# Optimization experiments

Hardware: AMD Instinct MI355X
Metric: run time of the kernel (lower is better)

## Reference

```python
import jax, jax.numpy as jnp
import numpy as np

H = W = 512
MAX_ID = 15          # instance ids 1..15 (0 = background)
N_SIGMA = 1
FG_WEIGHT = 1.0
W_INST, W_VAR, W_SEED = 1.0, 10.0, 1.0


def make_xym(h, w):
    # channel 0 varies along width (x), channel 1 along height (y), like the torch buffer
    xs = jnp.linspace(0.0, 1.0, 512)
    xm = jnp.broadcast_to(xs[None, None, :], (1, 512, 512))
    ym = jnp.broadcast_to(xs[None, :, None], (1, 512, 512))
    xym = jnp.concatenate([xm, ym], axis=0)
    return xym[:, :h, :w]


def lovasz_hinge_flat(logits, labels):
    # logits, labels: flat [P]; labels in {0,1} float
    signs = 2.0 * labels - 1.0
    errors = 1.0 - logits * signs
    perm = jnp.argsort(-errors)                 # descending
    errors_sorted = errors[perm]
    gt_sorted = labels[perm]
    gts = jnp.sum(gt_sorted)
    intersection = gts - jnp.cumsum(gt_sorted)
    union = gts + jnp.cumsum(1.0 - gt_sorted)
    jaccard = 1.0 - intersection / union
    jaccard = jnp.concatenate([jaccard[:1], jaccard[1:] - jaccard[:-1]])
    return jnp.sum(jax.nn.relu(errors_sorted) * jaccard)


def _per_image(pred_b, inst_b, lab_b, xym):
    spatial_emb = jnp.tanh(pred_b[0:2]) + xym          # (2,H,W)
    sigma = pred_b[2]                                  # (H,W), n_sigma=1
    seed_map = jax.nn.sigmoid(pred_b[3])               # (H,W)

    bg = (lab_b == 0)
    seed_bg = jnp.sum(jnp.where(bg, seed_map ** 2, 0.0))

    def per_inst(iid):
        m = (inst_b == iid).astype(pred_b.dtype)       # (H,W)
        cnt = jnp.sum(m)
        present = cnt > 0
        cnt_s = jnp.maximum(cnt, 1.0)
        # to_center=True: center from coordinate map
        center = jnp.sum(xym * m[None], axis=(1, 2)) / cnt_s            # (2,)
        sig_mean = jnp.sum(sigma * m) / cnt_s
        var_l = jnp.sum((sigma - jax.lax.stop_gradient(sig_mean)) ** 2 * m) / cnt_s
        s = jnp.exp(sig_mean * 10.0)
        d2 = jnp.sum((spatial_emb - center[:, None, None]) ** 2, axis=0)  # (H,W)
        dist = jnp.exp(-d2 * s)
        inst_l = lovasz_hinge_flat(dist.reshape(-1) * 2.0 - 1.0, m.reshape(-1))
        seed_l = jnp.sum((seed_map - jax.lax.stop_gradient(dist)) ** 2 * m)
        intra_l = 1.0 - jnp.sum(dist * m) / cnt_s
        return present, var_l, inst_l, seed_l, intra_l

    ids = jnp.arange(1, MAX_ID + 1)
    present, var_l, inst_l, seed_l, intra_l = jax.vmap(per_inst)(ids)
    pf = present.astype(pred_b.dtype)
    obj = jnp.sum(pf)
    obj_s = jnp.maximum(obj, 1.0)
    instance_loss = jnp.sum(inst_l * pf) / obj_s
    var_loss = jnp.sum(var_l * pf) / obj_s
    intra_loss = jnp.sum(intra_l * pf)          # NOT divided by obj_count (as in source)
    seed_loss = (seed_bg + FG_WEIGHT * jnp.sum(seed_l * pf)) / (H * W)
    return W_INST * instance_loss + W_VAR * var_loss + W_SEED * seed_loss + 5.0 * intra_loss


def setup_inputs() -> dict:
    key = jax.random.key(0)
    k1, k2, k3 = jax.random.split(key, 3)
    prediction = jax.random.normal(k1, (4, 4, H, W), dtype=jnp.float32)
    instances = jax.random.randint(k2, (4, H, W), 0, MAX_ID + 1, dtype=jnp.int32)
    labels = jax.random.randint(k3, (4, H, W), 0, 2, dtype=jnp.int32)
    return {"prediction": prediction, "instances": instances, "labels": labels}


def reference(prediction, instances, labels):
    xym = make_xym(prediction.shape[2], prediction.shape[3])
    per_b = jax.vmap(_per_image, in_axes=(0, 0, 0, None))(prediction, instances, labels, xym)
    return jnp.mean(per_b)
```

## Files before the change

kernel.cpp:

```cpp
#include <hip/hip_runtime.h>

#define HW     262144
#define NB     4
#define NID    15
#define KB     256
#define CHUNKS 128
#define PXC    (HW / CHUNKS)

#define WS_STATR  0
#define WS_SEEDBG 1024
#define WS_ACCR   1028
#define WS_LOV    1796
#define WS_CTRL   2048
#define WS_HIST   2048
#define HIST_U32  (NB * CHUNKS * NID * KB)
#define WS_EMBX   (WS_HIST + HIST_U32)
#define MAP_SZ    (NB * HW)
#define WS_EMBY   (WS_EMBX + MAP_SZ)
#define WS_SEEDM  (WS_EMBY + MAP_SZ)
#define WS_TOTAL  (WS_SEEDM + MAP_SZ)

__device__ __forceinline__ float rcp_fast(float x) { return __builtin_amdgcn_rcpf(x); }
__device__ __forceinline__ float fast_tanh(float x) {
    return 1.0f - 2.0f * rcp_fast(__expf(2.0f * x) + 1.0f);
}
__device__ __forceinline__ float fast_sigmoid(float x) {
    return rcp_fast(1.0f + __expf(-x));
}

__global__ __launch_bounds__(256) void zeroKernel(float* __restrict__ ws) {
    ws[blockIdx.x * 256 + threadIdx.x] = 0.f;
}

__global__ __launch_bounds__(256) void prepKernel(const float* __restrict__ pred,
                                                  const int* __restrict__ inst,
                                                  const int* __restrict__ lab,
                                                  float* __restrict__ ws) {
    __shared__ float s_acc[16][68];
    const int b   = blockIdx.y;
    const int tid = threadIdx.x;
    for (int j = tid; j < 16 * 68; j += 256) ((float*)s_acc)[j] = 0.f;
    __syncthreads();

    const int grp = tid >> 4;
    const int ib = b * HW;
    const float* p0 = pred + (((size_t)(b * 4 + 0)) << 18);
    const float* p1 = pred + (((size_t)(b * 4 + 1)) << 18);
    const float* p2 = pred + (((size_t)(b * 4 + 2)) << 18);
    const float* p3 = pred + (((size_t)(b * 4 + 3)) << 18);
    float* embx  = ws + WS_EMBX + ib;
    float* emby  = ws + WS_EMBY + ib;
    float* seedm = ws + WS_SEEDM + ib;
    const float inv511 = 1.0f / 511.0f;

    const int p = blockIdx.x * 1024 + tid * 4;
    const int4   i4 = *(const int4*)(inst + ib + p);
    const int4   l4 = *(const int4*)(lab + ib + p);
    const float4 a4 = *(const float4*)(p0 + p);
    const float4 b4 = *(const float4*)(p1 + p);
    const float4 g4 = *(const float4*)(p2 + p);
    const float4 t4 = *(const float4*)(p3 + p);
    const float xs0 = (float)(p & 511) * inv511;
    const float ys  = (float)(p >> 9) * inv511;

    float4 ex, ey, sd;
    ex.x = fast_tanh(a4.x) + xs0;
    ex.y = fast_tanh(a4.y) + xs0 + inv511;
    ex.z = fast_tanh(a4.z) + xs0 + 2.f * inv511;
    ex.w = fast_tanh(a4.w) + xs0 + 3.f * inv511;
    ey.x = fast_tanh(b4.x) + ys;
    ey.y = fast_tanh(b4.y) + ys;
    ey.z = fast_tanh(b4.z) + ys;
    ey.w = fast_tanh(b4.w) + ys;
    sd.x = fast_sigmoid(t4.x);
    sd.y = fast_sigmoid(t4.y);
    sd.z = fast_sigmoid(t4.z);
    sd.w = fast_sigmoid(t4.w);
    *(float4*)(embx + p)  = ex;
    *(float4*)(emby + p)  = ey;
    *(float4*)(seedm + p) = sd;

    float sbg = 0.f;
    sbg += (l4.x == 0) ? sd.x * sd.x : 0.f;
    sbg += (l4.y == 0) ? sd.y * sd.y : 0.f;
    sbg += (l4.z == 0) ? sd.z * sd.z : 0.f;
    sbg += (l4.w == 0) ? sd.w * sd.w : 0.f;

#define ACC_PX(IID, XS, SG)                                   \
    if ((IID) > 0) {                                          \
        float* a = &s_acc[grp][((IID) - 1) * 4];              \
        atomicAdd(a + 0, 1.f);                                \
        atomicAdd(a + 1, (XS));                               \
        atomicAdd(a + 2, ys);                                 \
        atomicAdd(a + 3, (SG));                               \
    }
    ACC_PX(i4.x, xs0, g4.x)
    ACC_PX(i4.y, xs0 + inv511, g4.y)
    ACC_PX(i4.z, xs0 + 2.f * inv511, g4.z)
    ACC_PX(i4.w, xs0 + 3.f * inv511, g4.w)
#undef ACC_PX

#pragma unroll
    for (int m = 32; m; m >>= 1) sbg += __shfl_xor(sbg, m, 64);
    if ((tid & 63) == 0) atomicAdd(&s_acc[grp][60], sbg);
    __syncthreads();

    if (tid < 61) {
        float tot = 0.f;
#pragma unroll
        for (int q = 0; q < 16; ++q) tot += s_acc[q][tid];
        if (tid < 60) atomicAdd(ws + WS_STATR + (blockIdx.x & 3) * 256 + b * 60 + tid, tot);
        else          atomicAdd(ws + WS_SEEDBG + b, tot);
    }
}

#define HCOPY_STRIDE (NID * KB + 1)
__global__ __launch_bounds__(256) void histKernel(const float* __restrict__ pred,
                                                  const int* __restrict__ inst,
                                                  float* __restrict__ ws) {
    __shared__ unsigned s_hist[4 * HCOPY_STRIDE];
    __shared__ float4   s_stat4[NID];
    __shared__ float    s_facc[8][48];

    const int b     = blockIdx.y;
    const int chunk = blockIdx.x;
    const int tid   = threadIdx.x;

    if (tid < NID) {
        float cnt = 0.f, sx = 0.f, sy = 0.f, ss = 0.f;
#pragma unroll
        for (int r = 0; r < 4; ++r) {
            const float* st = ws + WS_STATR + r * 256 + b * 60 + tid * 4;
            cnt += st[0]; sx += st[1]; sy += st[2]; ss += st[3];
        }
        float ic = rcp_fast(fmaxf(cnt, 1.f));
        float sigm = ss * ic;
        s_stat4[tid] = make_float4(sx * ic, sy * ic, sigm, __expf(10.f * sigm));
    }
    for (int j = tid; j < 4 * HCOPY_STRIDE; j += 256) s_hist[j] = 0u;
    for (int j = tid; j < 8 * 48; j += 256) ((float*)s_facc)[j] = 0.f;
    __syncthreads();

    float csx[NID], csy[NID], css[NID];
#pragma unroll
    for (int i = 0; i < NID; ++i) {
        float4 v = s_stat4[i];
        csx[i] = v.x; csy[i] = v.y; css[i] = v.w;
    }

    unsigned* myhist = &s_hist[((tid >> 4) & 3) * HCOPY_STRIDE];
    float* myfacc = s_facc[(tid >> 3) & 7];
    const int ib = b * HW;
    const float* sig   = pred + (((size_t)(b * 4 + 2)) << 18);
    const float* embx  = ws + WS_EMBX + ib;
    const float* emby  = ws + WS_EMBY + ib;
    const float* seedm = ws + WS_SEEDM + ib;

    auto doPx = [&](float exv, float eyv, float sdv, float gv, int iid) {
#pragma unroll
        for (int i = 0; i < NID; ++i) {
            float dx = exv - csx[i], dy = eyv - csy[i];
            float dist = __expf(-(dx * dx + dy * dy) * css[i]);
            float u1 = dist * (float)KB;
            bool m = (iid == i + 1);
            float bf = m ? ((float)KB - u1) : u1;
            int bk = min((int)bf, KB - 1);
            atomicAdd(&myhist[i * KB + bk], m ? 1u : 0x10000u);
        }
        if (iid > 0) {
            float4 st = s_stat4[iid - 1];
            float dx = exv - st.x, dy = eyv - st.y;
            float dist = __expf(-(dx * dx + dy * dy) * st.w);
            float dsg = gv - st.z;
            float e2 = sdv - dist;
            float* fa = &myfacc[(iid - 1) * 3];
            atomicAdd(fa + 0, dsg * dsg);
            atomicAdd(fa + 1, e2 * e2);
            atomicAdd(fa + 2, dist);
        }
    };

#pragma unroll
    for (int u = 0; u < 2; ++u) {
        const int p = chunk * PXC + u * 1024 + tid * 4;
        const int4   i4 = *(const int4*)(inst + ib + p);
        const float4 exq = *(const float4*)(embx + p);
        const float4 eyq = *(const float4*)(emby + p);
        const float4 sdq = *(const float4*)(seedm + p);
        const float4 gq  = *(const float4*)(sig + p);
        doPx(exq.x, eyq.x, sdq.x, gq.x, i4.x);
        doPx(exq.y, eyq.y, sdq.y, gq.y, i4.y);
        doPx(exq.z, eyq.z, sdq.z, gq.z, i4.z);
        doPx(exq.w, eyq.w, sdq.w, gq.w, i4.w);
    }
    __syncthreads();

    unsigned* dst = (unsigned*)(ws + WS_HIST) + (size_t)(b * CHUNKS + chunk) * (NID * KB);
    for (int j = tid; j < NID * KB; j += 256) {
        dst[j] = s_hist[j] + s_hist[HCOPY_STRIDE + j] +
                 s_hist[2 * HCOPY_STRIDE + j] + s_hist[3 * HCOPY_STRIDE + j];
    }

    if (tid < 45) {
        float tot = 0.f;
#pragma unroll
        for (int q = 0; q < 8; ++q) tot += s_facc[q][tid];
        atomicAdd(ws + WS_ACCR + (chunk & 3) * 192 + b * 48 + tid, tot);
    }
}

__global__ __launch_bounds__(256) void lovaszKernel(float* __restrict__ ws) {
    __shared__ unsigned s_pf[4][KB];
    __shared__ unsigned s_pb[4][KB];
    const int t = blockIdx.x;
    const int b = t / NID, i = t % NID;
    const int tid = threadIdx.x, wv = tid >> 6, lane = tid & 63;

    float G = 0.f;
#pragma unroll
    for (int r = 0; r < 4; ++r) G += ws[WS_STATR + r * 256 + b * 60 + i * 4];

    if (G > 0.f) {
        unsigned af0 = 0, af1 = 0, af2 = 0, af3 = 0;
        unsigned ab0 = 0, ab1 = 0, ab2 = 0, ab3 = 0;
        const unsigned* histU = (const unsigned*)(ws + WS_HIST);
        for (int k = 0; k < 32; ++k) {
            const int c = wv * 32 + k;
            const unsigned* hb = histU + ((size_t)(b * CHUNKS + c) * NID + i) * KB + lane * 4;
            uint4 q = *(const uint4*)hb;
            af0 += q.x & 0xffffu; ab0 += q.x >> 16;
            af1 += q.y & 0xffffu; ab1 += q.y >> 16;
            af2 += q.z & 0xffffu; ab2 += q.z >> 16;
            af3 += q.w & 0xffffu; ab3 += q.w >> 16;
        }
        s_pf[wv][lane * 4 + 0] = af0; s_pb[wv][lane * 4 + 0] = ab0;
        s_pf[wv][lane * 4 + 1] = af1; s_pb[wv][lane * 4 + 1] = ab1;
        s_pf[wv][lane * 4 + 2] = af2; s_pb[wv][lane * 4 + 2] = ab2;
        s_pf[wv][lane * 4 + 3] = af3; s_pb[wv][lane * 4 + 3] = ab3;
    }
    __syncthreads();

    float sum = 0.f;
    if (wv == 0 && G > 0.f) {
        float fgs[4], bgs[4];
#pragma unroll
        for (int q = 0; q < 4; ++q) {
            int k = lane * 4 + q;
            fgs[q] = (float)(s_pf[0][k] + s_pf[1][k] + s_pf[2][k] + s_pf[3][k]);
            bgs[q] = (float)(s_pb[0][k] + s_pb[1][k] + s_pb[2][k] + s_pb[3][k]);
        }
        float Fl = fgs[0] + fgs[1] + fgs[2] + fgs[3];
        float Bl = bgs[0] + bgs[1] + bgs[2] + bgs[3];
        float Fs = Fl, Bs = Bl;
#pragma unroll
        for (int d = 1; d < 64; d <<= 1) {
            float fu = __shfl_down(Fs, d, 64);
            float bu = __shfl_down(Bs, d, 64);
            if (lane + d < 64) { Fs += fu; Bs += bu; }
        }
        float F = Fs - Fl, B = Bs - Bl;
        float Jprev = 1.f - (G - F) * rcp_fast(G + B);
        const float ew = 2.f / (float)KB;
#pragma unroll
        for (int q = 3; q >= 0; --q) {
            F += fgs[q]; B += bgs[q];
            float J = 1.f - (G - F) * rcp_fast(G + B);
            float ek = ((float)(lane * 4 + q) + 0.5f) * ew;
            sum += ek * (J - Jprev);
            Jprev = J;
        }
#pragma unroll
        for (int m = 32; m; m >>= 1) sum += __shfl_xor(sum, m, 64);
    }
    if (tid == 0) ws[WS_LOV + t] = sum;
}

__global__ __launch_bounds__(64) void finalKernel(const float* __restrict__ ws,
                                                  float* __restrict__ out) {
    __shared__ float s_c[60][5];
    const int tid = threadIdx.x;
    if (tid < 60) {
        const int b = tid / NID, i = tid % NID;
        float cnt = 0.f, v = 0.f, sdl = 0.f, dm = 0.f;
#pragma unroll
        for (int r = 0; r < 4; ++r) {
            cnt += ws[WS_STATR + r * 256 + b * 60 + i * 4];
            const float* ac = ws + WS_ACCR + r * 192 + b * 48 + i * 3;
            v += ac[0]; sdl += ac[1]; dm += ac[2];
        }
        float pf = cnt > 0.f ? 1.f : 0.f;
        float ic = cnt > 0.f ? 1.f / cnt : 0.f;
        s_c[tid][0] = pf;
        s_c[tid][1] = pf * ws[WS_LOV + tid];
        s_c[tid][2] = pf * v * ic;
        s_c[tid][3] = pf * (1.f - dm * ic);
        s_c[tid][4] = pf * sdl;
    }
    __syncthreads();
    if (tid == 0) {
        float total = 0.f;
        for (int b = 0; b < NB; ++b) {
            float obj = 0.f, instl = 0.f, varl = 0.f, intral = 0.f, seedl = 0.f;
            for (int i = 0; i < NID; ++i) {
                const float* r = s_c[b * NID + i];
                obj += r[0]; instl += r[1]; varl += r[2]; intral += r[3]; seedl += r[4];
            }
            float objs = fmaxf(obj, 1.f);
            total += instl / objs
                   + 10.f * (varl / objs)
                   + (ws[WS_SEEDBG + b] + seedl) / (float)HW
                   + 5.f * intral;
        }
        out[0] = total * 0.25f;
    }
}

extern "C" void kernel_launch(void* const* d_in, const int* in_sizes, int n_in,
                              void* d_out, int out_size, void* d_ws, size_t ws_size,
                              hipStream_t stream) {
    const float* pred = (const float*)d_in[0];
    const int*   inst = (const int*)d_in[1];
    const int*   lab  = (const int*)d_in[2];
    float* ws  = (float*)d_ws;
    float* out = (float*)d_out;

    zeroKernel<<<WS_CTRL / 256, 256, 0, stream>>>(ws);
    prepKernel<<<dim3(256, NB), 256, 0, stream>>>(pred, inst, lab, ws);
    histKernel<<<dim3(CHUNKS, NB), 256, 0, stream>>>(pred, inst, ws);
    lovaszKernel<<<60, 256, 0, stream>>>(ws);
    finalKernel<<<1, 64, 0, stream>>>(ws, out);
}
```

Measured before the change: 79.68 us.

## Drop zero and final kernels via per-block partials and last-block ticket

Replaces the global float atomics into zeroed accumulators with per-block partial writes. Each consumer now reduces those partials itself, which removes the separate zeroing kernel. The final reduction is folded into the Lovasz kernel: a ticket counter picks the last block to compute the output, cutting two kernel launches. It adds redundant partial-sum reads in every hist block and depends on threadfence-based cross-block ordering.

```diff
diff --git a/kernel.cpp b/kernel.cpp
--- a/kernel.cpp
+++ b/kernel.cpp
@@ -7,12 +7,13 @@
 #define CHUNKS 128
 #define PXC    (HW / CHUNKS)
 
-#define WS_STATR  0
-#define WS_SEEDBG 1024
-#define WS_ACCR   1028
-#define WS_LOV    1796
-#define WS_CTRL   2048
-#define WS_HIST   2048
+#define WS_TICKET 0
+#define WS_GACC   4
+#define WS_SBGR   24
+#define WS_PART   64
+#define PART_STR  1024
+#define WS_FACC   65600
+#define WS_HIST   90432
 #define HIST_U32  (NB * CHUNKS * NID * KB)
 #define WS_EMBX   (WS_HIST + HIST_U32)
 #define MAP_SZ    (NB * HW)
@@ -27,10 +28,7 @@
 __device__ __forceinline__ float fast_sigmoid(float x) {
     return rcp_fast(1.0f + __expf(-x));
 }
-
-__global__ __launch_bounds__(256) void zeroKernel(float* __restrict__ ws) {
-    ws[blockIdx.x * 256 + threadIdx.x] = 0.f;
-}
+__device__ __forceinline__ float atomic_read(float* p) { return atomicAdd(p, 0.0f); }
 
 __global__ __launch_bounds__(256) void prepKernel(const float* __restrict__ pred,
                                                   const int* __restrict__ inst,
@@ -109,8 +107,11 @@
         float tot = 0.f;
 #pragma unroll
         for (int q = 0; q < 16; ++q) tot += s_acc[q][tid];
-        if (tid < 60) atomicAdd(ws + WS_STATR + (blockIdx.x & 3) * 256 + b * 60 + tid, tot);
-        else          atomicAdd(ws + WS_SEEDBG + b, tot);
+        ws[WS_PART + tid * PART_STR + b * 256 + blockIdx.x] = tot;
+    }
+    if (blockIdx.x == 0 && b == 0) {
+        if (tid < 20)       ws[WS_GACC + tid] = 0.f;
+        else if (tid == 20) ((unsigned*)ws)[WS_TICKET] = 0u;
     }
 }
 
@@ -121,24 +122,32 @@
     __shared__ unsigned s_hist[4 * HCOPY_STRIDE];
     __shared__ float4   s_stat4[NID];
     __shared__ float    s_facc[8][48];
+    __shared__ float    s_comp[61];
 
     const int b     = blockIdx.y;
     const int chunk = blockIdx.x;
     const int tid   = threadIdx.x;
-
-    if (tid < NID) {
-        float cnt = 0.f, sx = 0.f, sy = 0.f, ss = 0.f;
-#pragma unroll
-        for (int r = 0; r < 4; ++r) {
-            const float* st = ws + WS_STATR + r * 256 + b * 60 + tid * 4;
-            cnt += st[0]; sx += st[1]; sy += st[2]; ss += st[3];
-        }
-        float ic = rcp_fast(fmaxf(cnt, 1.f));
-        float sigm = ss * ic;
-        s_stat4[tid] = make_float4(sx * ic, sy * ic, sigm, __expf(10.f * sigm));
+    const int wv = tid >> 6, lane = tid & 63;
+
+    for (int c = wv; c < 61; c += 4) {
+        const float* pp = ws + WS_PART + c * PART_STR + b * 256;
+        float v = pp[lane] + pp[lane + 64] + pp[lane + 128] + pp[lane + 192];
+#pragma unroll
+        for (int m = 32; m; m >>= 1) v += __shfl_xor(v, m, 64);
+        if (lane == 0) s_comp[c] = v;
     }
     for (int j = tid; j < 4 * HCOPY_STRIDE; j += 256) s_hist[j] = 0u;
     for (int j = tid; j < 8 * 48; j += 256) ((float*)s_facc)[j] = 0.f;
+    __syncthreads();
+
+    if (tid < NID) {
+        float cnt = s_comp[tid * 4 + 0];
+        float ic = rcp_fast(fmaxf(cnt, 1.f));
+        float sigm = s_comp[tid * 4 + 3] * ic;
+        s_stat4[tid] = make_float4(s_comp[tid * 4 + 1] * ic, s_comp[tid * 4 + 2] * ic,
+                                   sigm, __expf(10.f * sigm));
+    }
+    if (chunk == 0 && tid == 16) ws[WS_SBGR + b] = s_comp[60];
     __syncthreads();
 
     float csx[NID], csy[NID], css[NID];
@@ -200,25 +209,46 @@
         dst[j] = s_hist[j] + s_hist[HCOPY_STRIDE + j] +
                  s_hist[2 * HCOPY_STRIDE + j] + s_hist[3 * HCOPY_STRIDE + j];
     }
-
     if (tid < 45) {
         float tot = 0.f;
 #pragma unroll
         for (int q = 0; q < 8; ++q) tot += s_facc[q][tid];
-        atomicAdd(ws + WS_ACCR + (chunk & 3) * 192 + b * 48 + tid, tot);
-    }
-}
-
-__global__ __launch_bounds__(256) void lovaszKernel(float* __restrict__ ws) {
+        ws[WS_FACC + (size_t)(b * CHUNKS + chunk) * 48 + tid] = tot;
+    }
+}
+
+__global__ __launch_bounds__(256) void lovaszKernel(float* __restrict__ ws,
+                                                    float* __restrict__ out) {
     __shared__ unsigned s_pf[4][KB];
     __shared__ unsigned s_pb[4][KB];
+    __shared__ float s4[4];
+    __shared__ float s_f[4][3];
     const int t = blockIdx.x;
     const int b = t / NID, i = t % NID;
     const int tid = threadIdx.x, wv = tid >> 6, lane = tid & 63;
 
-    float G = 0.f;
-#pragma unroll
-    for (int r = 0; r < 4; ++r) G += ws[WS_STATR + r * 256 + b * 60 + i * 4];
+    {
+        float g = ws[WS_PART + (i * 4) * PART_STR + b * 256 + tid];
+#pragma unroll
+        for (int m = 32; m; m >>= 1) g += __shfl_xor(g, m, 64);
+        if (lane == 0) s4[wv] = g;
+    }
+    {
+        float f0 = 0.f, f1 = 0.f, f2 = 0.f;
+        if (tid < CHUNKS) {
+            const float* fb = ws + WS_FACC + (size_t)(b * CHUNKS + tid) * 48 + i * 3;
+            f0 = fb[0]; f1 = fb[1]; f2 = fb[2];
+        }
+#pragma unroll
+        for (int m = 32; m; m >>= 1) {
+            f0 += __shfl_xor(f0, m, 64);
+            f1 += __shfl_xor(f1, m, 64);
+            f2 += __shfl_xor(f2, m, 64);
+        }
+        if (lane == 0) { s_f[wv][0] = f0; s_f[wv][1] = f1; s_f[wv][2] = f2; }
+    }
+    __syncthreads();
+    const float G = s4[0] + s4[1] + s4[2] + s4[3];
 
     if (G > 0.f) {
         unsigned af0 = 0, af1 = 0, af2 = 0, af3 = 0;
@@ -272,46 +302,40 @@
 #pragma unroll
         for (int m = 32; m; m >>= 1) sum += __shfl_xor(sum, m, 64);
     }
-    if (tid == 0) ws[WS_LOV + t] = sum;
-}
-
-__global__ __launch_bounds__(64) void finalKernel(const float* __restrict__ ws,
-                                                  float* __restrict__ out) {
-    __shared__ float s_c[60][5];
-    const int tid = threadIdx.x;
-    if (tid < 60) {
-        const int b = tid / NID, i = tid % NID;
-        float cnt = 0.f, v = 0.f, sdl = 0.f, dm = 0.f;
-#pragma unroll
-        for (int r = 0; r < 4; ++r) {
-            cnt += ws[WS_STATR + r * 256 + b * 60 + i * 4];
-            const float* ac = ws + WS_ACCR + r * 192 + b * 48 + i * 3;
-            v += ac[0]; sdl += ac[1]; dm += ac[2];
-        }
-        float pf = cnt > 0.f ? 1.f : 0.f;
-        float ic = cnt > 0.f ? 1.f / cnt : 0.f;
-        s_c[tid][0] = pf;
-        s_c[tid][1] = pf * ws[WS_LOV + tid];
-        s_c[tid][2] = pf * v * ic;
-        s_c[tid][3] = pf * (1.f - dm * ic);
-        s_c[tid][4] = pf * sdl;
-    }
-    __syncthreads();
+
+    if (tid == 0 && G > 0.f) {
+        float ic = rcp_fast(fmaxf(G, 1.f));
+        float F0 = s_f[0][0] + s_f[1][0] + s_f[2][0] + s_f[3][0];
+        float F1 = s_f[0][1] + s_f[1][1] + s_f[2][1] + s_f[3][1];
+        float F2 = s_f[0][2] + s_f[1][2] + s_f[2][2] + s_f[3][2];
+        float* ga = ws + WS_GACC + b * 5;
+        atomicAdd(ga + 0, 1.f);
+        atomicAdd(ga + 1, sum);
+        atomicAdd(ga + 2, F0 * ic);
+        atomicAdd(ga + 3, 1.f - F2 * ic);
+        atomicAdd(ga + 4, F1);
+    }
+    __threadfence();
     if (tid == 0) {
-        float total = 0.f;
-        for (int b = 0; b < NB; ++b) {
-            float obj = 0.f, instl = 0.f, varl = 0.f, intral = 0.f, seedl = 0.f;
-            for (int i = 0; i < NID; ++i) {
-                const float* r = s_c[b * NID + i];
-                obj += r[0]; instl += r[1]; varl += r[2]; intral += r[3]; seedl += r[4];
+        unsigned tk = atomicAdd((unsigned*)ws + WS_TICKET, 1u);
+        if (tk == 59u) {
+            float total = 0.f;
+            for (int bb = 0; bb < NB; ++bb) {
+                float* ga = ws + WS_GACC + bb * 5;
+                float obj   = atomic_read(ga + 0);
+                float instl = atomic_read(ga + 1);
+                float varl  = atomic_read(ga + 2);
+                float intral= atomic_read(ga + 3);
+                float seedl = atomic_read(ga + 4);
+                float sbg   = ws[WS_SBGR + bb];
+                float objs  = fmaxf(obj, 1.f);
+                total += instl / objs
+                       + 10.f * (varl / objs)
+                       + (sbg + seedl) / (float)HW
+                       + 5.f * intral;
             }
-            float objs = fmaxf(obj, 1.f);
-            total += instl / objs
-                   + 10.f * (varl / objs)
-                   + (ws[WS_SEEDBG + b] + seedl) / (float)HW
-                   + 5.f * intral;
-        }
-        out[0] = total * 0.25f;
+            out[0] = total * 0.25f;
+        }
     }
 }
 
@@ -324,9 +348,7 @@
     float* ws  = (float*)d_ws;
     float* out = (float*)d_out;
 
-    zeroKernel<<<WS_CTRL / 256, 256, 0, stream>>>(ws);
     prepKernel<<<dim3(256, NB), 256, 0, stream>>>(pred, inst, lab, ws);
     histKernel<<<dim3(CHUNKS, NB), 256, 0, stream>>>(pred, inst, ws);
-    lovaszKernel<<<60, 256, 0, stream>>>(ws);
-    finalKernel<<<1, 64, 0, stream>>>(ws, out);
-}
+    lovaszKernel<<<60, 256, 0, stream>>>(ws, out);
+}
```

Result: slower. 83.63 us (+5.0%).
